# Performance work log

Measured on AMD Instinct MI355X. Metric: run time of the kernel, lower is better.

Reference implementation:

```python
import jax, jax.numpy as jnp
import numpy as np

D = 1024
H = 16
DH = D // H


def setup_inputs() -> dict:
    key = jax.random.key(0)
    ks = jax.random.split(key, 9)
    s = 1.0 / np.sqrt(D)
    x = jax.random.normal(ks[0], (4, 2048, D), dtype=jnp.float32)
    Wq = jax.random.uniform(ks[1], (D, D), jnp.float32, -s, s)
    bq = jax.random.uniform(ks[2], (D,), jnp.float32, -s, s)
    Wk = jax.random.uniform(ks[3], (D, D), jnp.float32, -s, s)
    bk = jax.random.uniform(ks[4], (D,), jnp.float32, -s, s)
    Wv = jax.random.uniform(ks[5], (D, D), jnp.float32, -s, s)
    bv = jax.random.uniform(ks[6], (D,), jnp.float32, -s, s)
    Wo = jax.random.uniform(ks[7], (D, D), jnp.float32, -s, s)
    bo = jax.random.uniform(ks[8], (D,), jnp.float32, -s, s)
    return {"x": x, "Wq": Wq, "bq": bq, "Wk": Wk, "bk": bk,
            "Wv": Wv, "bv": bv, "Wo": Wo, "bo": bo}


def _split_heads(t):
    b, s, d = t.shape
    return t.reshape(b, s, H, DH).transpose(0, 2, 1, 3)  # (B,H,S,Dh)


def reference(x, Wq, bq, Wk, bk, Wv, bv, Wo, bo):
    # Self-attention: context = x
    q = _split_heads(x @ Wq.T + bq)
    k = _split_heads(x @ Wk.T + bk)
    v = _split_heads(x @ Wv.T + bv)
    scale = 1.0 / np.sqrt(DH).astype(np.float32)
    logits = jnp.einsum('bhqd,bhkd->bhqk', q, k) * scale
    attn = jax.nn.softmax(logits, axis=-1)
    out_h = jnp.einsum('bhqk,bhkd->bhqd', attn, v)  # (B,H,S,Dh)
    b, h, s, dh = out_h.shape
    out = out_h.transpose(0, 2, 1, 3).reshape(b, s, h * dh)
    return out @ Wo.T + bo
```

## Files before the change

kernel.cpp:

```cpp
#include <hip/hip_runtime.h>
#include <cstdint>
#include <cstddef>

typedef unsigned short u16;
typedef __attribute__((ext_vector_type(8))) short short8;
typedef __attribute__((ext_vector_type(4))) short sv4;
typedef __attribute__((ext_vector_type(4))) float f32x4;

__device__ __forceinline__ u16 f2bf(float f) {
  unsigned int u = __builtin_bit_cast(unsigned int, f);
  u += 0x7FFFu + ((u >> 16) & 1u);
  return (u16)(u >> 16);
}
__device__ __forceinline__ float bf2f(u16 v) {
  return __builtin_bit_cast(float, ((unsigned int)v) << 16);
}

__device__ __forceinline__ f32x4 mfma_16x16x16_bf16(sv4 a, sv4 b, f32x4 c) {
#if defined(__HIP_DEVICE_COMPILE__)
#if __has_builtin(__builtin_amdgcn_mfma_f32_16x16x16bf16_1k)
  return __builtin_amdgcn_mfma_f32_16x16x16bf16_1k(a, b, c, 0, 0, 0);
#elif __has_builtin(__builtin_amdgcn_mfma_f32_16x16x16_bf16)
  return __builtin_amdgcn_mfma_f32_16x16x16_bf16(a, b, c, 0, 0, 0);
#else
  asm volatile("v_mfma_f32_16x16x16_bf16 %0, %1, %2, %0\n\ts_nop 7\n\ts_nop 4"
               : "+v"(c) : "v"(a), "v"(b));
  return c;
#endif
#else
  (void)a; (void)b;
  return c;
#endif
}

#define GLD_LDS(g, l) __builtin_amdgcn_global_load_lds( \
    (const __attribute__((address_space(1))) void*)(g), \
    (__attribute__((address_space(3))) void*)(l), 16, 0, 0)

__global__ void detect_dtype(const u16* __restrict__ x, int* __restrict__ flag)
{
  const int lane = threadIdx.x;
  int hit = 0;
#pragma unroll
  for (int j = 0; j < 4; ++j) {
    float v = bf2f(x[lane * 4 + j]);
    if (!(v > -1000.f && v < 1000.f)) hit = 1;
  }
  unsigned long long any = __ballot(hit != 0);
  if (lane == 0) *flag = (any != 0ull) ? 1 : 0;
}

__global__ __launch_bounds__(256)
void convert_wb(const void* Wq, const void* Wk, const void* Wv, const void* Wo,
                const void* bq, const void* bk, const void* bv, const void* bo,
                u16* __restrict__ Wc, u16* __restrict__ bc, const int* __restrict__ flag)
{
  const int fp32 = *flag;
  const size_t base = ((size_t)blockIdx.x * 256 + threadIdx.x) * 8;
  const void* src; u16* dst; size_t local;
  if (base < (size_t)4 * 1048576) {
    const int sel = (int)(base >> 20);
    local = base & 1048575u;
    src = (sel == 0) ? Wq : (sel == 1) ? Wk : (sel == 2) ? Wv : Wo;
    dst = Wc + (size_t)sel * 1048576 + local;
  } else {
    const size_t rem = base - (size_t)4 * 1048576;
    const int sel = (int)(rem >> 10);
    local = rem & 1023u;
    src = (sel == 0) ? bq : (sel == 1) ? bk : (sel == 2) ? bv : bo;
    dst = bc + (size_t)sel * 1024 + local;
  }
  if (fp32) {
    const float* s = (const float*)src + local;
#pragma unroll
    for (int j = 0; j < 8; ++j) dst[j] = f2bf(s[j]);
  } else {
    *(short8*)dst = *(const short8*)((const u16*)src + local);
  }
}

__global__ __launch_bounds__(256)
void convert_x_off(const void* __restrict__ x, u16* __restrict__ dst,
                   const int* __restrict__ flag, int b)
{
  const int fp32 = *flag;
  const size_t base = ((size_t)blockIdx.x * 256 + threadIdx.x) * 8;
  const size_t src_e = (size_t)b * 2048 * 1024 + base;
  if (fp32) {
    const float* s = (const float*)x + src_e;
#pragma unroll
    for (int j = 0; j < 8; ++j) dst[base + j] = f2bf(s[j]);
  } else {
    *(short8*)(dst + base) = *(const short8*)((const u16*)x + src_e);
  }
}

__global__ __launch_bounds__(256)
void gemm_bt(const u16* __restrict__ A,
             const u16* __restrict__ B0, const u16* __restrict__ B1, const u16* __restrict__ B2,
             const u16* __restrict__ bias, u16* __restrict__ C, int Ntot, int K)
{
  __shared__ __align__(16) u16 Alds[128 * 32];
  __shared__ __align__(16) u16 Blds[128 * 32];
  const int tid  = threadIdx.x;
  const int wave = tid >> 6, lane = tid & 63;
  const int quad = lane >> 4, l15 = lane & 15;
  const int m0  = blockIdx.y * 128;
  const int n0g = blockIdx.x * 128;
  const int sel = n0g >> 10;
  const u16* Bm = (sel == 0) ? B0 : ((sel == 1) ? B1 : B2);
  const u16* bb = bias + (size_t)sel * 1024;
  const int n0 = n0g & 1023;
  const int wr = (wave >> 1) * 64, wc = (wave & 1) * 64;

  f32x4 acc[4][4] = {};
  const int srow = lane >> 2;
  const int skc  = (lane & 3) * 8;
  const u16* Ag = A  + (size_t)(m0 + srow) * K + skc;
  const u16* Bg = Bm + (size_t)(n0 + srow) * K + skc;

  for (int kt = 0; kt < K; kt += 32) {
    __syncthreads();
#pragma unroll
    for (int t = 0; t < 2; ++t) {
      const int seg = wave * 2 + t;
      GLD_LDS(Ag + (size_t)(seg * 16) * K + kt, Alds + seg * 512);
      GLD_LDS(Bg + (size_t)(seg * 16) * K + kt, Blds + seg * 512);
    }
    __syncthreads();

    short8 af[4], bfr[4];
#pragma unroll
    for (int i = 0; i < 4; ++i)
      af[i] = *(const short8*)&Alds[(wr + i * 16 + l15) * 32 + quad * 8];
#pragma unroll
    for (int j = 0; j < 4; ++j)
      bfr[j] = *(const short8*)&Blds[(wc + j * 16 + l15) * 32 + quad * 8];
#pragma unroll
    for (int i = 0; i < 4; ++i)
#pragma unroll
      for (int j = 0; j < 4; ++j)
        acc[i][j] = __builtin_amdgcn_mfma_f32_16x16x32_bf16(af[i], bfr[j], acc[i][j], 0, 0, 0);
  }

#pragma unroll
  for (int i = 0; i < 4; ++i) {
    const int mr = m0 + wr + i * 16 + quad * 4;
#pragma unroll
    for (int j = 0; j < 4; ++j) {
      const int ncl = wc + j * 16 + l15;
      const float bvv = bf2f(bb[n0 + ncl]);
#pragma unroll
      for (int r = 0; r < 4; ++r)
        C[(size_t)(mr + r) * Ntot + n0g + ncl] = f2bf(acc[i][j][r] + bvv);
    }
  }
}

__global__ __launch_bounds__(256)
void gemm_bt_out(const u16* __restrict__ A, const u16* __restrict__ Bm,
                 const u16* __restrict__ bias, void* __restrict__ C16,
                 void* __restrict__ C32, int Ntot, int K, const int* __restrict__ flag)
{
  __shared__ __align__(16) u16 Alds[128 * 32];
  __shared__ __align__(16) u16 Blds[128 * 32];
  const int tid  = threadIdx.x;
  const int wave = tid >> 6, lane = tid & 63;
  const int quad = lane >> 4, l15 = lane & 15;
  const int m0 = blockIdx.y * 128;
  const int n0 = blockIdx.x * 128;
  const int wr = (wave >> 1) * 64, wc = (wave & 1) * 64;

  f32x4 acc[4][4] = {};
  const int srow = lane >> 2;
  const int skc  = (lane & 3) * 8;
  const u16* Ag = A  + (size_t)(m0 + srow) * K + skc;
  const u16* Bg = Bm + (size_t)(n0 + srow) * K + skc;

  for (int kt = 0; kt < K; kt += 32) {
    __syncthreads();
#pragma unroll
    for (int t = 0; t < 2; ++t) {
      const int seg = wave * 2 + t;
      GLD_LDS(Ag + (size_t)(seg * 16) * K + kt, Alds + seg * 512);
      GLD_LDS(Bg + (size_t)(seg * 16) * K + kt, Blds + seg * 512);
    }
    __syncthreads();

    short8 af[4], bfr[4];
#pragma unroll
    for (int i = 0; i < 4; ++i)
      af[i] = *(const short8*)&Alds[(wr + i * 16 + l15) * 32 + quad * 8];
#pragma unroll
    for (int j = 0; j < 4; ++j)
      bfr[j] = *(const short8*)&Blds[(wc + j * 16 + l15) * 32 + quad * 8];
#pragma unroll
    for (int i = 0; i < 4; ++i)
#pragma unroll
      for (int j = 0; j < 4; ++j)
        acc[i][j] = __builtin_amdgcn_mfma_f32_16x16x32_bf16(af[i], bfr[j], acc[i][j], 0, 0, 0);
  }

  if (*flag != 0) {
    float* Cf = (float*)C32;
#pragma unroll
    for (int i = 0; i < 4; ++i) {
      const int mr = m0 + wr + i * 16 + quad * 4;
#pragma unroll
      for (int j = 0; j < 4; ++j) {
        const int ncl = wc + j * 16 + l15;
        const float bvv = bf2f(bias[n0 + ncl]);
#pragma unroll
        for (int r = 0; r < 4; ++r)
          Cf[(size_t)(mr + r) * Ntot + n0 + ncl] = acc[i][j][r] + bvv;
      }
    }
  } else {
    u16* Cb = (u16*)C16;
#pragma unroll
    for (int i = 0; i < 4; ++i) {
      const int mr = m0 + wr + i * 16 + quad * 4;
#pragma unroll
      for (int j = 0; j < 4; ++j) {
        const int ncl = wc + j * 16 + l15;
        const float bvv = bf2f(bias[n0 + ncl]);
#pragma unroll
        for (int r = 0; r < 4; ++r)
          Cb[(size_t)(mr + r) * Ntot + n0 + ncl] = f2bf(acc[i][j][r] + bvv);
      }
    }
  }
}

__global__ __launch_bounds__(256, 4)
void attn_s(const u16* __restrict__ QKV, u16* __restrict__ O)
{
  __shared__ __align__(16) u16 Klds[64 * 72];
  __shared__ __align__(16) unsigned int Vlds[64 * 32];
  const int tid  = threadIdx.x;
  const int wave = tid >> 6, lane = tid & 63;
  const int quad = lane >> 4, l15 = lane & 15;
  const int qt = blockIdx.x, h = blockIdx.y;
  const u16* QKVb = QKV + (size_t)blockIdx.z * 2048 * 3072;
  u16* Ob = O + (size_t)blockIdx.z * 2048 * 1024;
  const int q0 = qt * 128;
  const float SCL = 0.18033688011112042f;

  short8 qf[2][2];
  const u16* Qb = QKVb + (size_t)(q0 + wave * 32) * 3072 + h * 64;
#pragma unroll
  for (int rt = 0; rt < 2; ++rt)
#pragma unroll
    for (int kh = 0; kh < 2; ++kh)
      qf[rt][kh] = *(const short8*)(Qb + (size_t)(rt * 16 + l15) * 3072 + kh * 32 + quad * 8);

  f32x4 oaccT[4][2] = {};
  float lrow[2] = {};

  const int ksrow = tid >> 2;
  const int kscb  = (tid & 3) * 16;
  const int vkvp = lane & 31;
  const int vd0  = wave * 16 + (lane >> 5) * 8;

  const u16* Kb = QKVb + 1024 + h * 64;
  const u16* Vb = QKVb + 2048 + h * 64;

  for (int kv0 = 0; kv0 < 2048; kv0 += 64) {
    __syncthreads();
    {
      const u16* kp = Kb + (size_t)(kv0 + ksrow) * 3072 + kscb;
      *(short8*)&Klds[ksrow * 72 + kscb]     = *(const short8*)kp;
      *(short8*)&Klds[ksrow * 72 + kscb + 8] = *(const short8*)(kp + 8);

      const u16* v0p = Vb + (size_t)(kv0 + 2 * vkvp) * 3072 + vd0;
      short8 va = *(const short8*)v0p;
      short8 vb2 = *(const short8*)(v0p + 3072);
      const int kb = vkvp >> 1, kl = vkvp & 1;
#pragma unroll
      for (int j = 0; j < 8; ++j) {
        const int d = vd0 + j;
        Vlds[d * 32 + ((kb ^ (d & 15)) << 1) + kl] =
            ((unsigned int)(unsigned short)va[j]) |
            (((unsigned int)(unsigned short)vb2[j]) << 16);
      }
    }
    __syncthreads();

    f32x4 sacc[4][2] = {};
#pragma unroll
    for (int kh = 0; kh < 2; ++kh) {
      short8 kf[4];
#pragma unroll
      for (int ct = 0; ct < 4; ++ct)
        kf[ct] = *(const short8*)&Klds[(ct * 16 + l15) * 72 + kh * 32 + quad * 8];
#pragma unroll
      for (int ct = 0; ct < 4; ++ct)
#pragma unroll
        for (int rt = 0; rt < 2; ++rt)
          sacc[ct][rt] = __builtin_amdgcn_mfma_f32_16x16x32_bf16(kf[ct], qf[rt][kh], sacc[ct][rt], 0, 0, 0);
    }

    sv4 p16[4][2];
#pragma unroll
    for (int rt = 0; rt < 2; ++rt) {
      float rs = 0.f;
#pragma unroll
      for (int ct = 0; ct < 4; ++ct) {
#pragma unroll
        for (int r = 0; r < 4; ++r) {
          const float p = __builtin_amdgcn_exp2f(sacc[ct][rt][r] * SCL);
          rs += p;
          p16[ct][rt][r] = (short)f2bf(p);
        }
      }
      rs += __shfl_xor(rs, 16, 64);
      rs += __shfl_xor(rs, 32, 64);
      lrow[rt] += rs;
    }

#pragma unroll
    for (int ct = 0; ct < 4; ++ct) {
#pragma unroll
      for (int dt = 0; dt < 4; ++dt) {
        const int d = dt * 16 + l15;
        const int idx = d * 32 + (((ct * 4 + quad) ^ (d & 15)) << 1);
        const sv4 vfr = *(const sv4*)&Vlds[idx];
#pragma unroll
        for (int rt = 0; rt < 2; ++rt)
          oaccT[dt][rt] = mfma_16x16x16_bf16(vfr, p16[ct][rt], oaccT[dt][rt]);
      }
    }
  }

#pragma unroll
  for (int rt = 0; rt < 2; ++rt) {
    const float inv = 1.f / lrow[rt];
    u16* Op = Ob + (size_t)(q0 + wave * 32 + rt * 16 + l15) * 1024 + h * 64;
#pragma unroll
    for (int dt = 0; dt < 4; ++dt) {
      sv4 ov;
#pragma unroll
      for (int r = 0; r < 4; ++r) ov[r] = (short)f2bf(oaccT[dt][rt][r] * inv);
      *(sv4*)(Op + dt * 16 + quad * 4) = ov;
    }
  }
}

extern "C" void kernel_launch(void* const* d_in, const int* in_sizes, int n_in,
                              void* d_out, int out_size, void* d_ws, size_t ws_size,
                              hipStream_t stream)
{
  int* flag = (int*)d_ws;
  u16* Wc   = (u16*)((char*)d_ws + 256);
  u16* bc   = Wc + (size_t)4 * 1048576;
  char* after_wb = (char*)(bc + 4096);

  detect_dtype<<<1, 64, 0, stream>>>((const u16*)d_in[0], flag);
  convert_wb<<<2050, 256, 0, stream>>>(d_in[1], d_in[3], d_in[5], d_in[7],
                                       d_in[2], d_in[4], d_in[6], d_in[8],
                                       Wc, bc, flag);

  const size_t need_batched =
      (size_t)(after_wb - (char*)d_ws) + ((size_t)8192 * 3072 + (size_t)8192 * 1024) * 2;

  if (ws_size >= need_batched) {
    u16* QKV = (u16*)after_wb;
    u16* xO  = QKV + (size_t)8192 * 3072;

    convert_x_off<<<4096, 256, 0, stream>>>(d_in[0], xO, flag, 0);
    gemm_bt<<<dim3(24, 64), 256, 0, stream>>>(xO, Wc, Wc + 1048576, Wc + 2097152,
                                              bc, QKV, 3072, 1024);
    attn_s<<<dim3(16, 16, 4), 256, 0, stream>>>(QKV, xO);
    gemm_bt_out<<<dim3(8, 64), 256, 0, stream>>>(xO, Wc + (size_t)3 * 1048576,
                                                 bc + 3 * 1024, d_out, d_out,
                                                 1024, 1024, flag);
  } else {
    u16* xc   = (u16*)after_wb;
    u16* QKVb = xc + (size_t)2048 * 1024;
    u16* Obb  = QKVb + (size_t)2048 * 3072;
    for (int b = 0; b < 4; ++b) {
      convert_x_off<<<1024, 256, 0, stream>>>(d_in[0], xc, flag, b);
      gemm_bt<<<dim3(24, 16), 256, 0, stream>>>(xc, Wc, Wc + 1048576, Wc + 2097152,
                                                bc, QKVb, 3072, 1024);
      attn_s<<<dim3(16, 16, 1), 256, 0, stream>>>(QKVb, Obb);
      void* outb16 = (void*)((char*)d_out + (size_t)b * 2048 * 1024 * 2);
      void* outb32 = (void*)((char*)d_out + (size_t)b * 2048 * 1024 * 4);
      gemm_bt_out<<<dim3(8, 16), 256, 0, stream>>>(Obb, Wc + (size_t)3 * 1048576,
                                                   bc + 3 * 1024, outb16, outb32,
                                                   1024, 1024, flag);
    }
  }
}
```

Measured before the change: 313.7 us.

## Fold softmax scale into Wq/bq, pack bf16 conversions, swap GEMM grid order

```diff
diff --git a/kernel.cpp b/kernel.cpp
--- a/kernel.cpp
+++ b/kernel.cpp
@@ -6,6 +6,8 @@
 typedef __attribute__((ext_vector_type(8))) short short8;
 typedef __attribute__((ext_vector_type(4))) short sv4;
 typedef __attribute__((ext_vector_type(4))) float f32x4;
+typedef __attribute__((ext_vector_type(2))) unsigned int u32x2;
+typedef __attribute__((ext_vector_type(4))) unsigned int u32x4;
 
 __device__ __forceinline__ u16 f2bf(float f) {
   unsigned int u = __builtin_bit_cast(unsigned int, f);
@@ -14,6 +16,16 @@
 }
 __device__ __forceinline__ float bf2f(u16 v) {
   return __builtin_bit_cast(float, ((unsigned int)v) << 16);
+}
+
+__device__ __forceinline__ unsigned int pk_bf16(float a, float b) {
+#if defined(__HIP_DEVICE_COMPILE__) && __has_builtin(__builtin_amdgcn_cvt_pk_bf16_f32)
+  typedef __attribute__((ext_vector_type(2))) __bf16 bf16x2;
+  bf16x2 r = __builtin_amdgcn_cvt_pk_bf16_f32(a, b);
+  return __builtin_bit_cast(unsigned int, r);
+#else
+  return (unsigned int)f2bf(a) | ((unsigned int)f2bf(b) << 16);
+#endif
 }
 
 __device__ __forceinline__ f32x4 mfma_16x16x16_bf16(sv4 a, sv4 b, f32x4 c) {
@@ -37,6 +49,8 @@
     (const __attribute__((address_space(1))) void*)(g), \
     (__attribute__((address_space(3))) void*)(l), 16, 0, 0)
 
+#define QSCL 0.18033688011112042f
+
 __global__ void detect_dtype(const u16* __restrict__ x, int* __restrict__ flag)
 {
   const int lane = threadIdx.x;
@@ -57,25 +71,37 @@
 {
   const int fp32 = *flag;
   const size_t base = ((size_t)blockIdx.x * 256 + threadIdx.x) * 8;
-  const void* src; u16* dst; size_t local;
+  const void* src; u16* dst; size_t local; int sel;
   if (base < (size_t)4 * 1048576) {
-    const int sel = (int)(base >> 20);
+    sel = (int)(base >> 20);
     local = base & 1048575u;
     src = (sel == 0) ? Wq : (sel == 1) ? Wk : (sel == 2) ? Wv : Wo;
     dst = Wc + (size_t)sel * 1048576 + local;
   } else {
     const size_t rem = base - (size_t)4 * 1048576;
-    const int sel = (int)(rem >> 10);
+    sel = (int)(rem >> 10);
     local = rem & 1023u;
     src = (sel == 0) ? bq : (sel == 1) ? bk : (sel == 2) ? bv : bo;
     dst = bc + (size_t)sel * 1024 + local;
   }
+  const float scale = (sel == 0) ? QSCL : 1.0f;
   if (fp32) {
     const float* s = (const float*)src + local;
-#pragma unroll
-    for (int j = 0; j < 8; ++j) dst[j] = f2bf(s[j]);
+    u32x4 w;
+#pragma unroll
+    for (int j = 0; j < 4; ++j) w[j] = pk_bf16(s[2 * j] * scale, s[2 * j + 1] * scale);
+    *(short8*)dst = __builtin_bit_cast(short8, w);
   } else {
-    *(short8*)dst = *(const short8*)((const u16*)src + local);
+    const u16* s = (const u16*)src + local;
+    if (sel == 0) {
+      u32x4 w;
+#pragma unroll
+      for (int j = 0; j < 4; ++j)
+        w[j] = pk_bf16(bf2f(s[2 * j]) * scale, bf2f(s[2 * j + 1]) * scale);
+      *(short8*)dst = __builtin_bit_cast(short8, w);
+    } else {
+      *(short8*)dst = *(const short8*)s;
+    }
   }
 }
 
@@ -88,8 +114,10 @@
   const size_t src_e = (size_t)b * 2048 * 1024 + base;
   if (fp32) {
     const float* s = (const float*)x + src_e;
-#pragma unroll
-    for (int j = 0; j < 8; ++j) dst[base + j] = f2bf(s[j]);
+    u32x4 w;
+#pragma unroll
+    for (int j = 0; j < 4; ++j) w[j] = pk_bf16(s[2 * j], s[2 * j + 1]);
+    *(short8*)(dst + base) = __builtin_bit_cast(short8, w);
   } else {
     *(short8*)(dst + base) = *(const short8*)((const u16*)x + src_e);
   }
@@ -105,8 +133,8 @@
   const int tid  = threadIdx.x;
   const int wave = tid >> 6, lane = tid & 63;
   const int quad = lane >> 4, l15 = lane & 15;
-  const int m0  = blockIdx.y * 128;
-  const int n0g = blockIdx.x * 128;
+  const int m0  = blockIdx.x * 128;
+  const int n0g = blockIdx.y * 128;
   const int sel = n0g >> 10;
   const u16* Bm = (sel == 0) ? B0 : ((sel == 1) ? B1 : B2);
   const u16* bb = bias + (size_t)sel * 1024;
@@ -167,8 +195,8 @@
   const int tid  = threadIdx.x;
   const int wave = tid >> 6, lane = tid & 63;
   const int quad = lane >> 4, l15 = lane & 15;
-  const int m0 = blockIdx.y * 128;
-  const int n0 = blockIdx.x * 128;
+  const int m0 = blockIdx.x * 128;
+  const int n0 = blockIdx.y * 128;
   const int wr = (wave >> 1) * 64, wc = (wave & 1) * 64;
 
   f32x4 acc[4][4] = {};
@@ -244,7 +272,6 @@
   const u16* QKVb = QKV + (size_t)blockIdx.z * 2048 * 3072;
   u16* Ob = O + (size_t)blockIdx.z * 2048 * 1024;
   const int q0 = qt * 128;
-  const float SCL = 0.18033688011112042f;
 
   short8 qf[2][2];
   const u16* Qb = QKVb + (size_t)(q0 + wave * 32) * 3072 + h * 64;
@@ -306,12 +333,15 @@
       float rs = 0.f;
 #pragma unroll
       for (int ct = 0; ct < 4; ++ct) {
-#pragma unroll
-        for (int r = 0; r < 4; ++r) {
-          const float p = __builtin_amdgcn_exp2f(sacc[ct][rt][r] * SCL);
-          rs += p;
-          p16[ct][rt][r] = (short)f2bf(p);
-        }
+        float p0 = __builtin_amdgcn_exp2f(sacc[ct][rt][0]);
+        float p1 = __builtin_amdgcn_exp2f(sacc[ct][rt][1]);
+        float p2 = __builtin_amdgcn_exp2f(sacc[ct][rt][2]);
+        float p3 = __builtin_amdgcn_exp2f(sacc[ct][rt][3]);
+        rs += (p0 + p1) + (p2 + p3);
+        u32x2 pw;
+        pw[0] = pk_bf16(p0, p1);
+        pw[1] = pk_bf16(p2, p3);
+        p16[ct][rt] = __builtin_bit_cast(sv4, pw);
       }
       rs += __shfl_xor(rs, 16, 64);
       rs += __shfl_xor(rs, 32, 64);
@@ -338,10 +368,10 @@
     u16* Op = Ob + (size_t)(q0 + wave * 32 + rt * 16 + l15) * 1024 + h * 64;
 #pragma unroll
     for (int dt = 0; dt < 4; ++dt) {
-      sv4 ov;
-#pragma unroll
-      for (int r = 0; r < 4; ++r) ov[r] = (short)f2bf(oaccT[dt][rt][r] * inv);
-      *(sv4*)(Op + dt * 16 + quad * 4) = ov;
+      u32x2 ow;
+      ow[0] = pk_bf16(oaccT[dt][rt][0] * inv, oaccT[dt][rt][1] * inv);
+      ow[1] = pk_bf16(oaccT[dt][rt][2] * inv, oaccT[dt][rt][3] * inv);
+      *(sv4*)(Op + dt * 16 + quad * 4) = __builtin_bit_cast(sv4, ow);
     }
   }
 }
@@ -368,10 +398,10 @@
     u16* xO  = QKV + (size_t)8192 * 3072;
 
     convert_x_off<<<4096, 256, 0, stream>>>(d_in[0], xO, flag, 0);
-    gemm_bt<<<dim3(24, 64), 256, 0, stream>>>(xO, Wc, Wc + 1048576, Wc + 2097152,
+    gemm_bt<<<dim3(64, 24), 256, 0, stream>>>(xO, Wc, Wc + 1048576, Wc + 2097152,
                                               bc, QKV, 3072, 1024);
     attn_s<<<dim3(16, 16, 4), 256, 0, stream>>>(QKV, xO);
-    gemm_bt_out<<<dim3(8, 64), 256, 0, stream>>>(xO, Wc + (size_t)3 * 1048576,
+    gemm_bt_out<<<dim3(64, 8), 256, 0, stream>>>(xO, Wc + (size_t)3 * 1048576,
                                                  bc + 3 * 1024, d_out, d_out,
                                                  1024, 1024, flag);
   } else {
@@ -380,12 +410,12 @@
     u16* Obb  = QKVb + (size_t)2048 * 3072;
     for (int b = 0; b < 4; ++b) {
       convert_x_off<<<1024, 256, 0, stream>>>(d_in[0], xc, flag, b);
-      gemm_bt<<<dim3(24, 16), 256, 0, stream>>>(xc, Wc, Wc + 1048576, Wc + 2097152,
+      gemm_bt<<<dim3(16, 24), 256, 0, stream>>>(xc, Wc, Wc + 1048576, Wc + 2097152,
                                                 bc, QKVb, 3072, 1024);
       attn_s<<<dim3(16, 16, 1), 256, 0, stream>>>(QKVb, Obb);
       void* outb16 = (void*)((char*)d_out + (size_t)b * 2048 * 1024 * 2);
       void* outb32 = (void*)((char*)d_out + (size_t)b * 2048 * 1024 * 4);
-      gemm_bt_out<<<dim3(8, 16), 256, 0, stream>>>(Obb, Wc + (size_t)3 * 1048576,
+      gemm_bt_out<<<dim3(16, 8), 256, 0, stream>>>(Obb, Wc + (size_t)3 * 1048576,
                                                    bc + 3 * 1024, outb16, outb32,
                                                    1024, 1024, flag);
     }
```

Measured after the change: 311.5 us. About the same (-0.7%).
